# Performance work log

Hardware: AMD Instinct MI355X
Metric: run time of the kernel (lower is better)

Reference implementation:

```python
import jax, jax.numpy as jnp
import numpy as np

DECAY = 0.1  # P['decay']


def setup_inputs() -> dict:
    key = jax.random.key(0)
    k0, k1, k2, k3, k4 = jax.random.split(key, 5)
    N, B, T = 512, 64, 1024
    hidden_0 = jax.random.normal(k0, (N,), dtype=jnp.float32)
    Batch_Input = jax.random.normal(k1, (B, T, N), dtype=jnp.float32)
    # scale recurrent weight ~1/sqrt(N) so the leaky-tanh dynamics stay bounded
    W = jax.random.normal(k2, (N, N), dtype=jnp.float32) / np.sqrt(N).astype(np.float32)
    Gw = jax.random.normal(k3, (2, N), dtype=jnp.float32)
    Gb = jax.random.normal(k4, (2,), dtype=jnp.float32)
    return {"hidden_0": hidden_0, "Batch_Input": Batch_Input, "W": W, "Gw": Gw, "Gb": Gb}


def reference(hidden_0, Batch_Input, W, Gw, Gb):
    B, T, N = Batch_Input.shape
    h0 = jnp.broadcast_to(hidden_0[None, :], (B, N))  # repeat over batch
    xs = jnp.swapaxes(Batch_Input, 0, 1)  # [T, B, N] for scan over time

    def step(h, x):
        # h_new = (1-d)*h + d*(tanh(h) @ W^T + x)   (einsum 'ab,cb->ca')
        h_new = (1.0 - DECAY) * h + DECAY * (jnp.tanh(h) @ W.T + x)
        return h_new, jnp.tanh(h_new)

    _, hidden_t = jax.lax.scan(step, h0, xs)  # hidden_t: [T, B, N]
    geometry = hidden_t @ Gw.T + Gb  # [T, B, 2]
    return jnp.swapaxes(hidden_t, 0, 1), jnp.swapaxes(geometry, 0, 1)
```

## Files before the change

### kernel.cpp

```cpp
#include <hip/hip_runtime.h>
#include <hip/hip_fp16.h>
#include <cmath>

#define RN 512
#define RT 1024
#define RB 64
#define SMEM_BYTES (131072 + 320)

typedef _Float16 half2v __attribute__((ext_vector_type(2)));

__device__ __forceinline__ float fast_tanh(float x) {
    float e = __expf(2.0f * x);
    return 1.0f - 2.0f / (e + 1.0f);
}
__device__ __forceinline__ unsigned pack2(float a, float b) {
    return (unsigned)__half_as_ushort(__float2half(a)) |
           ((unsigned)__half_as_ushort(__float2half(b)) << 16);
}
__device__ __forceinline__ unsigned pkrtz(float a, float b) {
    auto h = __builtin_amdgcn_cvt_pkrtz(a, b);
    return __builtin_bit_cast(unsigned, h);
}
__device__ __forceinline__ float dot2(unsigned wa, unsigned tb, float acc) {
    half2v a = __builtin_bit_cast(half2v, wa);
    half2v b = __builtin_bit_cast(half2v, tb);
    return __builtin_amdgcn_fdot2(a, b, acc, false);
}
#define D2Q(acc, wq, tq) \
    acc = dot2((wq).x, (tq).x, acc); acc = dot2((wq).y, (tq).y, acc); \
    acc = dot2((wq).z, (tq).z, acc); acc = dot2((wq).w, (tq).w, acc);

__global__ void __launch_bounds__(512, 1) rnn_step_kernel(
    const float* __restrict__ h0,
    const float* __restrict__ X,
    const uint4* __restrict__ Wpk,
    const float* __restrict__ tanh0,
    float* __restrict__ outH,
    unsigned* __restrict__ ctr,
    unsigned* __restrict__ xcdctr)
{
    extern __shared__ unsigned char smem[];
    uint4*    Wl    = (uint4*)smem;
    unsigned* ownpk = (unsigned*)(smem + 131072);
    int*      bc    = (int*)(smem + 131072 + 256);

    const int tid = threadIdx.x;
    if (tid == 0) {
        unsigned xcd;
        asm volatile("s_getreg_b32 %0, hwreg(HW_REG_XCC_ID)" : "=s"(xcd));
        xcd &= 7u;
        unsigned rank = __hip_atomic_fetch_add(&xcdctr[xcd], 1u,
                            __ATOMIC_RELAXED, __HIP_MEMORY_SCOPE_AGENT) & 31u;
        int slot = (int)(xcd * 32u + rank);
        bc[0] = slot >> 2;
        bc[1] = slot & 3;
    }
    __syncthreads();
    const int batch = bc[0], part = bc[1];

    {
        const uint4* src = Wpk + part * 8192;
        #pragma unroll
        for (int i = 0; i < 16; ++i)
            Wl[i * 512 + tid] = src[i * 512 + tid];
    }

    const int rg = tid >> 4;
    const int kc = tid & 15;
    const int row0 = part * 128 + rg * 4;

    float4 h = {0, 0, 0, 0};
    if (kc == 0) {
        h = *reinterpret_cast<const float4*>(h0 + row0);
        float t0 = tanhf(h.x), t1 = tanhf(h.y), t2 = tanhf(h.z), t3 = tanhf(h.w);
        ownpk[2 * rg]     = pack2(t0, t1);
        ownpk[2 * rg + 1] = pack2(t2, t3);
    }

    unsigned* gctr = ctr + batch * 32;
    __syncthreads();

    #pragma unroll 1
    for (int t = 0; t < RT; ++t) {
        float acc0 = 0.f, acc1 = 0.f, acc2 = 0.f, acc3 = 0.f;
        {
            uint4 th = *reinterpret_cast<const uint4*>(&ownpk[4 * kc]);
            uint4 wq0 = Wl[(part * 4 + 0) * 512 + tid];
            uint4 wq1 = Wl[(part * 4 + 1) * 512 + tid];
            uint4 wq2 = Wl[(part * 4 + 2) * 512 + tid];
            uint4 wq3 = Wl[(part * 4 + 3) * 512 + tid];
            D2Q(acc0, wq0, th) D2Q(acc1, wq1, th)
            D2Q(acc2, wq2, th) D2Q(acc3, wq3, th)
        }
        float4 xv = {0, 0, 0, 0};
        if (kc == 0)
            xv = *reinterpret_cast<const float4*>(&X[((size_t)batch * RT + t) * RN + row0]);

        if (tid == 0 && t > 0) {
            const unsigned tgt = 4u * (unsigned)t;
            while (__hip_atomic_load(gctr, __ATOMIC_RELAXED,
                                     __HIP_MEMORY_SCOPE_AGENT) < tgt)
                __builtin_amdgcn_s_sleep(1);
        }
        __syncthreads();

        const float* srcR = (t == 0) ? tanh0
            : &outH[((size_t)batch * RT + (t - 1)) * RN];
        #pragma unroll
        for (int bb = 0; bb < 3; ++bb) {
            const int b = bb + (bb >= part);
            const int ko = b * 128 + kc * 8;
            float4 f0 = *reinterpret_cast<const float4*>(srcR + ko);
            float4 f1 = *reinterpret_cast<const float4*>(srcR + ko + 4);
            uint4 tv = make_uint4(pkrtz(f0.x, f0.y), pkrtz(f0.z, f0.w),
                                  pkrtz(f1.x, f1.y), pkrtz(f1.z, f1.w));
            uint4 wq0 = Wl[(b * 4 + 0) * 512 + tid];
            uint4 wq1 = Wl[(b * 4 + 1) * 512 + tid];
            uint4 wq2 = Wl[(b * 4 + 2) * 512 + tid];
            uint4 wq3 = Wl[(b * 4 + 3) * 512 + tid];
            D2Q(acc0, wq0, tv) D2Q(acc1, wq1, tv)
            D2Q(acc2, wq2, tv) D2Q(acc3, wq3, tv)
        }

        #pragma unroll
        for (int m = 1; m <= 8; m <<= 1) {
            acc0 += __shfl_xor(acc0, m);
            acc1 += __shfl_xor(acc1, m);
            acc2 += __shfl_xor(acc2, m);
            acc3 += __shfl_xor(acc3, m);
        }

        if (kc == 0) {
            h.x = 0.9f * h.x + 0.1f * (acc0 + xv.x);
            h.y = 0.9f * h.y + 0.1f * (acc1 + xv.y);
            h.z = 0.9f * h.z + 0.1f * (acc2 + xv.z);
            h.w = 0.9f * h.w + 0.1f * (acc3 + xv.w);
            float t0 = fast_tanh(h.x), t1 = fast_tanh(h.y);
            float t2 = fast_tanh(h.z), t3 = fast_tanh(h.w);
            *reinterpret_cast<float4*>(&outH[((size_t)batch * RT + t) * RN + row0]) =
                make_float4(t0, t1, t2, t3);
            ownpk[2 * rg]     = pack2(t0, t1);
            ownpk[2 * rg + 1] = pack2(t2, t3);
        }

        __syncthreads();
        if (tid == 0)
            __hip_atomic_fetch_add(gctr, 1u, __ATOMIC_RELAXED,
                                   __HIP_MEMORY_SCOPE_AGENT);
    }
}

__global__ void pack_w(const float* __restrict__ W, uint4* __restrict__ Wpk)
{
    int o = blockIdx.x * blockDim.x + threadIdx.x;
    if (o >= 32768) return;
    int part = o >> 13;
    int b    = (o >> 11) & 3;
    int i    = (o >> 9) & 3;
    int tid  = o & 511;
    int row  = part * 128 + (tid >> 4) * 4 + i;
    int k0   = b * 128 + (tid & 15) * 8;
    const float* s = W + (size_t)row * RN + k0;
    uint4 v;
    v.x = pack2(s[0], s[1]); v.y = pack2(s[2], s[3]);
    v.z = pack2(s[4], s[5]); v.w = pack2(s[6], s[7]);
    Wpk[o] = v;
}

__global__ void geom_kernel(const float* __restrict__ hid,
                            const float* __restrict__ Gw,
                            const float* __restrict__ Gb,
                            float* __restrict__ geo)
{
    const int wid  = (blockIdx.x * blockDim.x + threadIdx.x) >> 6;
    const int lane = threadIdx.x & 63;
    if (wid >= RB * RT) return;
    const float* rowp = hid + (size_t)wid * RN;
    float g0 = 0.f, g1 = 0.f;
    #pragma unroll
    for (int j = 0; j < 8; ++j) {
        float v = rowp[lane + 64 * j];
        g0 = fmaf(v, Gw[lane + 64 * j], g0);
        g1 = fmaf(v, Gw[RN + lane + 64 * j], g1);
    }
    #pragma unroll
    for (int m = 32; m >= 1; m >>= 1) {
        g0 += __shfl_xor(g0, m);
        g1 += __shfl_xor(g1, m);
    }
    if (lane == 0) {
        geo[(size_t)wid * 2]     = g0 + Gb[0];
        geo[(size_t)wid * 2 + 1] = g1 + Gb[1];
    }
}

__global__ void init_misc(const float* __restrict__ h0,
                          float* __restrict__ tanh0,
                          unsigned* __restrict__ ctr,
                          unsigned* __restrict__ xcdctr)
{
    int i = blockIdx.x * blockDim.x + threadIdx.x;
    if (i < RN) tanh0[i] = tanhf(h0[i]);
    if (i < RB * 32) ctr[i] = 0u;
    if (i < 8) xcdctr[i] = 0u;
}

extern "C" void kernel_launch(void* const* d_in, const int* in_sizes, int n_in,
                              void* d_out, int out_size, void* d_ws, size_t ws_size,
                              hipStream_t stream)
{
    const float* h0 = (const float*)d_in[0];
    const float* X  = (const float*)d_in[1];
    const float* W  = (const float*)d_in[2];
    const float* Gw = (const float*)d_in[3];
    const float* Gb = (const float*)d_in[4];

    float* outH = (float*)d_out;
    float* geo  = outH + (size_t)RB * RT * RN;

    float*    tanh0  = (float*)d_ws;
    unsigned* ctr    = (unsigned*)d_ws + RN;
    unsigned* xcdctr = ctr + RB * 32;
    uint4*    Wpk    = (uint4*)(((uintptr_t)(xcdctr + 8) + 15) & ~(uintptr_t)15);

    (void)hipFuncSetAttribute((const void*)rnn_step_kernel,
                              hipFuncAttributeMaxDynamicSharedMemorySize, SMEM_BYTES);

    pack_w<<<64, 512, 0, stream>>>(W, Wpk);
    init_misc<<<8, 512, 0, stream>>>(h0, tanh0, ctr, xcdctr);

    void* kargs[] = { (void*)&h0, (void*)&X, (void*)&Wpk, (void*)&tanh0,
                      (void*)&outH, (void*)&ctr, (void*)&xcdctr };
    (void)hipLaunchCooperativeKernel(rnn_step_kernel, dim3(256), dim3(512),
                                     kargs, SMEM_BYTES, stream);

    geom_kernel<<<(RB * RT * 64 + 255) / 256, 256, 0, stream>>>(outH, Gw, Gb, geo);
}
```

Measured before the change: 2.078 ms.

## Signal step completion from last wave, prefetch next X, use DPP reductions

Each wave now waits for its own global stores, then bumps a shared-memory counter. The last of the 8 waves to arrive publishes the global step counter, so the signal goes out before the trailing barrier rather than after it. The X slice for the next timestep is loaded one step ahead, taking that load off the critical path. The 16-lane shuffle reduction is replaced with DPP row operations. Together these aim to shorten the per-step cross-block dependency latency. The cost is extra LDS atomics and a new ordering scheme that relies on s_waitcnt for visibility.

```diff
diff --git a/kernel.cpp b/kernel.cpp
--- a/kernel.cpp
+++ b/kernel.cpp
@@ -25,6 +25,18 @@
     half2v a = __builtin_bit_cast(half2v, wa);
     half2v b = __builtin_bit_cast(half2v, tb);
     return __builtin_amdgcn_fdot2(a, b, acc, false);
+}
+template <int CTRL>
+__device__ __forceinline__ float dpp_add(float x) {
+    int p = __builtin_amdgcn_update_dpp(0, __float_as_int(x), CTRL, 0xf, 0xf, true);
+    return x + __int_as_float(p);
+}
+__device__ __forceinline__ float red16(float x) {
+    x = dpp_add<0xB1>(x);
+    x = dpp_add<0x4E>(x);
+    x = dpp_add<0x141>(x);
+    x = dpp_add<0x140>(x);
+    return x;
 }
 #define D2Q(acc, wq, tq) \
     acc = dot2((wq).x, (tq).x, acc); acc = dot2((wq).y, (tq).y, acc); \
@@ -43,6 +55,7 @@
     uint4*    Wl    = (uint4*)smem;
     unsigned* ownpk = (unsigned*)(smem + 131072);
     int*      bc    = (int*)(smem + 131072 + 256);
+    unsigned* lctr  = (unsigned*)(smem + 131072 + 264);
 
     const int tid = threadIdx.x;
     if (tid == 0) {
@@ -54,6 +67,7 @@
         int slot = (int)(xcd * 32u + rank);
         bc[0] = slot >> 2;
         bc[1] = slot & 3;
+        *lctr = 0u;
     }
     __syncthreads();
     const int batch = bc[0], part = bc[1];
@@ -70,11 +84,13 @@
     const int row0 = part * 128 + rg * 4;
 
     float4 h = {0, 0, 0, 0};
+    float4 xv = {0, 0, 0, 0};
     if (kc == 0) {
         h = *reinterpret_cast<const float4*>(h0 + row0);
         float t0 = tanhf(h.x), t1 = tanhf(h.y), t2 = tanhf(h.z), t3 = tanhf(h.w);
         ownpk[2 * rg]     = pack2(t0, t1);
         ownpk[2 * rg + 1] = pack2(t2, t3);
+        xv = *reinterpret_cast<const float4*>(&X[(size_t)batch * RT * RN + row0]);
     }
 
     unsigned* gctr = ctr + batch * 32;
@@ -82,6 +98,12 @@
 
     #pragma unroll 1
     for (int t = 0; t < RT; ++t) {
+        float4 xn = {0, 0, 0, 0};
+        if (kc == 0) {
+            const int tn = (t + 1 < RT) ? t + 1 : t;
+            xn = *reinterpret_cast<const float4*>(&X[((size_t)batch * RT + tn) * RN + row0]);
+        }
+
         float acc0 = 0.f, acc1 = 0.f, acc2 = 0.f, acc3 = 0.f;
         {
             uint4 th = *reinterpret_cast<const uint4*>(&ownpk[4 * kc]);
@@ -92,9 +114,6 @@
             D2Q(acc0, wq0, th) D2Q(acc1, wq1, th)
             D2Q(acc2, wq2, th) D2Q(acc3, wq3, th)
         }
-        float4 xv = {0, 0, 0, 0};
-        if (kc == 0)
-            xv = *reinterpret_cast<const float4*>(&X[((size_t)batch * RT + t) * RN + row0]);
 
         if (tid == 0 && t > 0) {
             const unsigned tgt = 4u * (unsigned)t;
@@ -122,13 +141,8 @@
             D2Q(acc2, wq2, tv) D2Q(acc3, wq3, tv)
         }
 
-        #pragma unroll
-        for (int m = 1; m <= 8; m <<= 1) {
-            acc0 += __shfl_xor(acc0, m);
-            acc1 += __shfl_xor(acc1, m);
-            acc2 += __shfl_xor(acc2, m);
-            acc3 += __shfl_xor(acc3, m);
-        }
+        acc0 = red16(acc0); acc1 = red16(acc1);
+        acc2 = red16(acc2); acc3 = red16(acc3);
 
         if (kc == 0) {
             h.x = 0.9f * h.x + 0.1f * (acc0 + xv.x);
@@ -143,10 +157,16 @@
             ownpk[2 * rg + 1] = pack2(t2, t3);
         }
 
+        asm volatile("s_waitcnt vmcnt(0)" ::: "memory");
+        if ((tid & 63) == 0) {
+            unsigned a = __hip_atomic_fetch_add(lctr, 1u, __ATOMIC_RELAXED,
+                                                __HIP_MEMORY_SCOPE_WORKGROUP);
+            if ((a & 7u) == 7u)
+                __hip_atomic_fetch_add(gctr, 1u, __ATOMIC_RELAXED,
+                                       __HIP_MEMORY_SCOPE_AGENT);
+        }
         __syncthreads();
-        if (tid == 0)
-            __hip_atomic_fetch_add(gctr, 1u, __ATOMIC_RELAXED,
-                                   __HIP_MEMORY_SCOPE_AGENT);
+        xv = xn;
     }
 }
 
```

Result: faster. 2.034 ms (-2.1%).
